# Performance work log

Hardware: AMD Instinct MI355X
Metric: run time of the kernel (lower is better)

## Reference

```python
import jax, jax.numpy as jnp
import numpy as np

B, S, D, H = 4, 1024, 1024, 16
HD = D // H  # head dim 64
EPS = 1e-12

def setup_inputs() -> dict:
    key = jax.random.key(0)
    ks = jax.random.split(key, 10)
    sc = 1.0 / np.sqrt(D)
    return {
        "eeg": jax.random.normal(ks[0], (B, S, D), jnp.float32),
        "pic": jax.random.normal(ks[1], (B, S, D), jnp.float32),
        "Wk": jax.random.normal(ks[2], (D, D), jnp.float32) * sc,
        "bk": jnp.zeros((D,), jnp.float32),
        "Wq": jax.random.normal(ks[3], (D, D), jnp.float32) * sc,
        "bq": jnp.zeros((D,), jnp.float32),
        "Wv": jax.random.normal(ks[4], (D, D), jnp.float32) * sc,
        "bv": jnp.zeros((D,), jnp.float32),
        "Wd": jax.random.normal(ks[5], (D, D), jnp.float32) * sc,
        "bd": jnp.zeros((D,), jnp.float32),
        "ln_w": jnp.ones((D,), jnp.float32),
        "ln_b": jnp.zeros((D,), jnp.float32),
    }

def _heads(x):  # [B,S,D] -> [B,H,S,HD]
    return x.reshape(B, S, H, HD).transpose(0, 2, 1, 3)

def reference(eeg, pic, Wk, bk, Wq, bq, Wv, bv, Wd, bd, ln_w, ln_b):
    k = _heads(eeg @ Wk + bk)
    q = _heads(pic @ Wq + bq)
    v = _heads(pic @ Wv + bv)
    scores = jnp.einsum('bhqd,bhkd->bhqk', q, k) / jnp.sqrt(jnp.float32(HD))
    probs = jax.nn.softmax(scores, axis=-1)  # dropout = identity (eval mode)
    ctx = jnp.einsum('bhqk,bhkd->bhqd', probs, v)
    ctx = ctx.transpose(0, 2, 1, 3).reshape(B, S, D)
    h = ctx @ Wd + bd  # out_dropout = identity (eval)
    x = h + pic
    u = x.mean(-1, keepdims=True)
    s = ((x - u) ** 2).mean(-1, keepdims=True)
    x = (x - u) / jnp.sqrt(s + EPS)
    return ln_w * x + ln_b
```

## Files before the change

### kernel.cpp

```cpp
#include <hip/hip_runtime.h>
#include <hip/hip_bf16.h>

#define BB 4
#define SS 1024
#define DD 1024
#define HH 16
#define HD 64
#define MM (BB * SS)
#define LN_EPS 1e-12f

typedef unsigned short u16;
typedef __attribute__((ext_vector_type(8))) short bf16x8;
typedef __attribute__((ext_vector_type(4))) float f32x4;
typedef __attribute__((ext_vector_type(4))) unsigned short u16x4;
typedef __attribute__((ext_vector_type(8))) unsigned short u16x8;

__device__ __forceinline__ u16 f2bf(float f) {
    __hip_bfloat16 h = __float2bfloat16(f);
    u16 r; __builtin_memcpy(&r, &h, 2); return r;
}
__device__ __forceinline__ float bf2f(u16 u) {
    unsigned v = ((unsigned)u) << 16;
    float f; __builtin_memcpy(&f, &v, 4); return f;
}

typedef const __attribute__((address_space(1))) unsigned int* gas1_t;
typedef __attribute__((address_space(3))) unsigned int* las3_t;
__device__ __forceinline__ void gload16(const void* g, void* s) {
    __builtin_amdgcn_global_load_lds((gas1_t)g, (las3_t)s, 16, 0, 0);
}

__device__ __forceinline__ void vmw0() {
    asm volatile("s_waitcnt vmcnt(0)" ::: "memory");
    __builtin_amdgcn_sched_barrier(0);
}
__device__ __forceinline__ void vmw2() {
    asm volatile("s_waitcnt vmcnt(2)" ::: "memory");
    __builtin_amdgcn_sched_barrier(0);
}
__device__ __forceinline__ void vmw4() {
    asm volatile("s_waitcnt vmcnt(4)" ::: "memory");
    __builtin_amdgcn_sched_barrier(0);
}

__global__ __launch_bounds__(256) void conv2_bf16(
    const float* __restrict__ a, const float* __restrict__ c,
    u16* __restrict__ oa, u16* __restrict__ oc)
{
    const float* in = blockIdx.y ? c : a;
    u16* out = blockIdx.y ? oc : oa;
    size_t i = ((size_t)blockIdx.x * 256 + threadIdx.x) * 8;
    float4 x = *(const float4*)(in + i);
    float4 y = *(const float4*)(in + i + 4);
    u16x8 o;
    o[0]=f2bf(x.x); o[1]=f2bf(x.y); o[2]=f2bf(x.z); o[3]=f2bf(x.w);
    o[4]=f2bf(y.x); o[5]=f2bf(y.y); o[6]=f2bf(y.z); o[7]=f2bf(y.w);
    *(u16x8*)(out + i) = o;
}

__global__ __launch_bounds__(256) void transpose_w4(
    const float* __restrict__ W0, const float* __restrict__ W1,
    const float* __restrict__ W2, const float* __restrict__ W3,
    u16* __restrict__ T0, u16* __restrict__ T1,
    u16* __restrict__ T2, u16* __restrict__ T3)
{
    const int z = blockIdx.z;
    const float* W = (z==0)?W0:(z==1)?W1:(z==2)?W2:W3;
    u16* Wt = (z==0)?T0:(z==1)?T1:(z==2)?T2:T3;

    __shared__ float Ls[64][65];
    const int t = threadIdx.x;
    const int k0 = blockIdx.x * 64, n0 = blockIdx.y * 64;
    #pragma unroll
    for (int i = 0; i < 4; ++i) {
        int r = (t >> 4) + i * 16, c = (t & 15) * 4;
        float4 v = *(const float4*)&W[(size_t)(k0 + r) * DD + n0 + c];
        Ls[r][c] = v.x; Ls[r][c+1] = v.y; Ls[r][c+2] = v.z; Ls[r][c+3] = v.w;
    }
    __syncthreads();
    #pragma unroll
    for (int i = 0; i < 2; ++i) {
        int n = (t >> 3) + i * 32, kc = (t & 7) * 8;
        u16x8 o;
        #pragma unroll
        for (int j = 0; j < 8; ++j) o[j] = f2bf(Ls[kc + j][n]);
        *(u16x8*)&Wt[(size_t)(n0 + n) * DD + k0 + kc] = o;
    }
}

template<int TRANS>
__device__ __forceinline__ void do_phase(
    const u16* Lcur, int wm, int wn, int g, int lr, int mh, int kh, f32x4* acc)
{
    const char* base = (const char*)Lcur;
    bf16x8 af[4], bfr[4];
    #pragma unroll
    for (int i = 0; i < 4; ++i) {
        int row = wm * 128 + mh * 64 + i * 16 + lr;
        af[i] = *(const bf16x8*)(base + row * 128 + ((kh * 4 + g) ^ (row & 7)) * 16);
    }
    #pragma unroll
    for (int i = 0; i < 4; ++i) {
        int row = wn * 64 + i * 16 + lr;
        bfr[i] = *(const bf16x8*)(base + 32768 + row * 128 + ((kh * 4 + g) ^ (row & 7)) * 16);
    }
    __builtin_amdgcn_s_setprio(1);
    #pragma unroll
    for (int i = 0; i < 4; ++i)
        #pragma unroll
        for (int j = 0; j < 4; ++j) {
            int mi = mh * 4 + i;
            if (TRANS)
                acc[j * 8 + mi] = __builtin_amdgcn_mfma_f32_16x16x32_bf16(
                    bfr[j], af[i], acc[j * 8 + mi], 0, 0, 0);
            else
                acc[mi * 4 + j] = __builtin_amdgcn_mfma_f32_16x16x32_bf16(
                    af[i], bfr[j], acc[mi * 4 + j], 0, 0, 0);
        }
    __builtin_amdgcn_s_setprio(0);
}

template<int TRANS>
__device__ __forceinline__ void gemm256_8ph(
    const u16* __restrict__ A, const u16* __restrict__ Bt,
    int bm, int bn, u16* Ls, f32x4* acc)
{
    const int tid = threadIdx.x;
    const int w = tid >> 6, l = tid & 63, g = l >> 4, lr = l & 15;
    const int wm = w >> 2, wn = w & 3;

    const int srow = tid >> 3;
    const int sgc = (tid & 7) ^ (srow & 7);
    const u16* Ag = A + (size_t)(bm + srow) * DD + sgc * 8;
    const u16* Bg = Bt + (size_t)(bn + srow) * DD + sgc * 8;

#define STA(buf, r, k0) gload16(Ag + (size_t)(r) * 64 * DD + (k0), (buf) + (r) * 4096 + w * 512)
#define STB(buf, r, k0) gload16(Bg + (size_t)(r) * 64 * DD + (k0), (buf) + 16384 + (r) * 4096 + w * 512)

    STB(Ls, 0, 0); STB(Ls, 1, 0);
    STB(Ls, 2, 0); STB(Ls, 3, 0);
    STA(Ls, 0, 0); STA(Ls, 2, 0);
    STA(Ls, 1, 0); STA(Ls, 3, 0);

    #pragma unroll 2
    for (int t = 0; t < 16; ++t) {
        const int cur = t & 1;
        const u16* cb = Ls + cur * 32768;
        u16* nb = Ls + (cur ^ 1) * 32768;
        const int nk = (t + 1) * 64;
        const bool last = (t == 15);

        vmw2();
        __builtin_amdgcn_s_barrier();
        if (!last) { STB(nb, 0, nk); STB(nb, 1, nk); }
        do_phase<TRANS>(cb, wm, wn, g, lr, 0, 0, acc);

        __builtin_amdgcn_s_barrier();
        if (!last) { STB(nb, 2, nk); STB(nb, 3, nk); }
        do_phase<TRANS>(cb, wm, wn, g, lr, 0, 1, acc);

        if (last) vmw0(); else vmw4();
        __builtin_amdgcn_s_barrier();
        if (!last) { STA(nb, 0, nk); STA(nb, 2, nk); }
        do_phase<TRANS>(cb, wm, wn, g, lr, 1, 0, acc);

        __builtin_amdgcn_s_barrier();
        if (!last) { STA(nb, 1, nk); STA(nb, 3, nk); }
        do_phase<TRANS>(cb, wm, wn, g, lr, 1, 1, acc);
    }
#undef STA
#undef STB
}

__global__ __launch_bounds__(512, 2) void gemm_qkv(
    const u16* __restrict__ Ae, const u16* __restrict__ Ap,
    const u16* __restrict__ Bk, const u16* __restrict__ Bq, const u16* __restrict__ Bv,
    const float* __restrict__ bk, const float* __restrict__ bq, const float* __restrict__ bv,
    u16* __restrict__ Kb, u16* __restrict__ Qb, u16* __restrict__ VtG)
{
    const int i = (int)blockIdx.x;
    const int x = i & 7, j = i >> 3;
    const int sel = j >> 3, inner = j & 7;
    const int bm = (x * 2 + (inner & 1)) * 256;
    const int bn = (inner >> 1) * 256;

    const u16* A  = sel ? Ap : Ae;
    const u16* Bt = (sel == 0) ? Bk : (sel == 1) ? Bq : Bv;
    const float* bias = (sel == 0) ? bk : (sel == 1) ? bq : bv;
    const float alpha = (sel == 1) ? 0.180336880111120f : 1.0f;

    __shared__ __align__(16) u16 Ls[2 * 32768];

    f32x4 acc[32];
    #pragma unroll
    for (int k = 0; k < 32; ++k) { f32x4 z = {0,0,0,0}; acc[k] = z; }

    const int tid = threadIdx.x;
    const int w = tid >> 6, l = tid & 63, g = l >> 4, lr = l & 15;
    const int wm = w >> 2, wn = w & 3;

    if (sel == 2) {
        gemm256_8ph<1>(A, Bt, bm, bn, Ls, acc);
        #pragma unroll
        for (int ni = 0; ni < 4; ++ni)
            #pragma unroll
            for (int r = 0; r < 4; ++r) {
                int n = bn + wn * 64 + ni * 16 + g * 4 + r;
                float bb = bias[n];
                #pragma unroll
                for (int mi = 0; mi < 8; ++mi) {
                    int m = bm + wm * 128 + mi * 16 + lr;
                    VtG[(size_t)n * MM + m] = f2bf(acc[ni * 8 + mi][r] + bb);
                }
            }
    } else {
        gemm256_8ph<0>(A, Bt, bm, bn, Ls, acc);
        u16* C = sel ? Qb : Kb;
        float b4[4];
        #pragma unroll
        for (int ni = 0; ni < 4; ++ni) b4[ni] = bias[bn + wn * 64 + ni * 16 + lr];
        #pragma unroll
        for (int mi = 0; mi < 8; ++mi)
            #pragma unroll
            for (int ni = 0; ni < 4; ++ni)
                #pragma unroll
                for (int r = 0; r < 4; ++r) {
                    int row = bm + wm * 128 + mi * 16 + g * 4 + r;
                    int col = bn + wn * 64 + ni * 16 + lr;
                    C[(size_t)row * DD + col] = f2bf(alpha * (acc[mi * 4 + ni][r] + b4[ni]));
                }
    }
}

template<int TRANS>
__device__ __forceinline__ void gemm128_loop(
    const u16* __restrict__ A, const u16* __restrict__ Bt,
    int bm, int bn, u16* As, u16* Bs, f32x4 (&acc)[4][4])
{
    const int tid = threadIdx.x;
    const int w = tid >> 6, l = tid & 63, g = l >> 4, lr = l & 15;
    const int wm = w >> 1, wn = w & 1;

    const int srow = tid >> 3, ss = tid & 7;
    const int sgc = ss ^ (srow & 7);
    const u16* Ag = A + (size_t)(bm + srow) * DD + sgc * 8;
    const u16* Bg = Bt + (size_t)(bn + srow) * DD + sgc * 8;

    for (int k0 = 0; k0 < DD; k0 += 64) {
        #pragma unroll
        for (int rr = 0; rr < 4; ++rr)
            gload16(Ag + (size_t)rr * 32 * DD + k0, As + (rr * 256 + w * 64) * 8);
        #pragma unroll
        for (int rr = 0; rr < 4; ++rr)
            gload16(Bg + (size_t)rr * 32 * DD + k0, Bs + (rr * 256 + w * 64) * 8);
        __syncthreads();

        #pragma unroll
        for (int kh = 0; kh < 2; ++kh) {
            bf16x8 af[4], bfr[4];
            #pragma unroll
            for (int mi = 0; mi < 4; ++mi) {
                int row = wm * 64 + mi * 16 + lr;
                af[mi] = *(const bf16x8*)((const char*)As + row * 128 +
                                          ((kh * 4 + g) ^ (row & 7)) * 16);
            }
            #pragma unroll
            for (int ni = 0; ni < 4; ++ni) {
                int row = wn * 64 + ni * 16 + lr;
                bfr[ni] = *(const bf16x8*)((const char*)Bs + row * 128 +
                                           ((kh * 4 + g) ^ (row & 7)) * 16);
            }
            #pragma unroll
            for (int mi = 0; mi < 4; ++mi)
                #pragma unroll
                for (int ni = 0; ni < 4; ++ni) {
                    if (TRANS)
                        acc[ni][mi] = __builtin_amdgcn_mfma_f32_16x16x32_bf16(
                            bfr[ni], af[mi], acc[ni][mi], 0, 0, 0);
                    else
                        acc[mi][ni] = __builtin_amdgcn_mfma_f32_16x16x32_bf16(
                            af[mi], bfr[ni], acc[mi][ni], 0, 0, 0);
                }
        }
        __syncthreads();
    }
}

__global__ __launch_bounds__(256) void gemm_plain(
    const u16* __restrict__ A, const u16* __restrict__ Bt,
    const float* __restrict__ bias, u16* __restrict__ C)
{
    const int i = (int)blockIdx.x;
    const int x = i & 7, j = i >> 3;
    const int bn = (j >> 2) * 128;
    const int bm = (x * 4 + (j & 3)) * 128;

    __shared__ __align__(16) u16 As[128 * 64];
    __shared__ __align__(16) u16 Bs[128 * 64];

    f32x4 acc[4][4];
    #pragma unroll
    for (int a = 0; a < 4; ++a)
        #pragma unroll
        for (int b = 0; b < 4; ++b) { f32x4 z = {0,0,0,0}; acc[a][b] = z; }

    gemm128_loop<0>(A, Bt, bm, bn, As, Bs, acc);

    const int tid = threadIdx.x;
    const int w = tid >> 6, l = tid & 63, g = l >> 4, lr = l & 15;
    const int wm = w >> 1, wn = w & 1;
    float b4[4];
    #pragma unroll
    for (int ni = 0; ni < 4; ++ni) b4[ni] = bias[bn + wn * 64 + ni * 16 + lr];
    #pragma unroll
    for (int mi = 0; mi < 4; ++mi)
        #pragma unroll
        for (int ni = 0; ni < 4; ++ni)
            #pragma unroll
            for (int r = 0; r < 4; ++r) {
                int row = bm + wm * 64 + mi * 16 + g * 4 + r;
                int col = bn + wn * 64 + ni * 16 + lr;
                C[(size_t)row * DD + col] = f2bf(acc[mi][ni][r] + b4[ni]);
            }
}

__global__ __launch_bounds__(512) void attn_mfma(
    const u16* __restrict__ Q, const u16* __restrict__ K,
    const u16* __restrict__ Vt, u16* __restrict__ O)
{
    const int tid = threadIdx.x;
    const int w = tid >> 6, l = tid & 63, g = l >> 4, lr = l & 15;
    int bid = (int)blockIdx.x;
    bid = (bid & 7) * 64 + (bid >> 3);
    const int qb = bid & 7, h = (bid >> 3) & 15, b = bid >> 7;
    const size_t qrow0 = (size_t)b * SS + qb * 128;
    const size_t kv0 = (size_t)b * SS;
    const int hc = h * HD;

    __shared__ __align__(16) u16 Ks[2][64 * 64];
    __shared__ __align__(16) u16 Vs[2][64 * 64];
    __shared__ __align__(16) u16 Ps[8][16 * 72];

    const int srow = tid >> 3, ss = tid & 7;
    const int sgc = ss ^ (srow & 7);
    const u16* kg = K + (kv0 + srow) * DD + hc + sgc * 8;
    const u16* vg = Vt + (size_t)(hc + srow) * MM + kv0 + sgc * 8;

    bf16x8 qf[2];
    {
        const u16* qp = Q + (qrow0 + w * 16 + lr) * DD + hc + g * 8;
        qf[0] = *(const bf16x8*)(qp);
        qf[1] = *(const bf16x8*)(qp + 32);
    }

    f32x4 acc[4];
    #pragma unroll
    for (int dt = 0; dt < 4; ++dt) { f32x4 z = {0,0,0,0}; acc[dt] = z; }
    float m_run = -1e30f, l_run = 0.f;

    gload16(kg, &Ks[0][w * 512]);
    gload16(vg, &Vs[0][w * 512]);
    __syncthreads();

    for (int kb = 0; kb < SS / 64; ++kb) {
        const int cur = kb & 1;
        if (kb < SS / 64 - 1) {
            gload16(kg + (size_t)(kb + 1) * 64 * DD, &Ks[cur ^ 1][w * 512]);
            gload16(vg + (size_t)(kb + 1) * 64, &Vs[cur ^ 1][w * 512]);
        }
        const char* kbase = (const char*)&Ks[cur][0];
        const char* vbase = (const char*)&Vs[cur][0];

        f32x4 st[4];
        __builtin_amdgcn_s_setprio(1);
        #pragma unroll
        for (int kt = 0; kt < 4; ++kt) {
            int row = kt * 16 + lr;
            const char* rb = kbase + row * 128;
            bf16x8 k0 = *(const bf16x8*)(rb + ((0 + g) ^ (row & 7)) * 16);
            bf16x8 k1 = *(const bf16x8*)(rb + ((4 + g) ^ (row & 7)) * 16);
            f32x4 z = {0,0,0,0};
            z = __builtin_amdgcn_mfma_f32_16x16x32_bf16(k0, qf[0], z, 0, 0, 0);
            z = __builtin_amdgcn_mfma_f32_16x16x32_bf16(k1, qf[1], z, 0, 0, 0);
            st[kt] = z;
        }
        __builtin_amdgcn_s_setprio(0);

        float tmax = -1e30f;
        #pragma unroll
        for (int kt = 0; kt < 4; ++kt)
            #pragma unroll
            for (int r = 0; r < 4; ++r) tmax = fmaxf(tmax, st[kt][r]);
        tmax = fmaxf(tmax, __shfl_xor(tmax, 16));
        tmax = fmaxf(tmax, __shfl_xor(tmax, 32));

        if (!__all(tmax <= m_run + 8.f)) {
            float m_new = fmaxf(m_run, tmax);
            float sc = exp2f(m_run - m_new);
            m_run = m_new;
            l_run *= sc;
            float scq[4];
            #pragma unroll
            for (int r = 0; r < 4; ++r) scq[r] = __shfl(sc, g * 4 + r);
            #pragma unroll
            for (int dt = 0; dt < 4; ++dt)
                #pragma unroll
                for (int r = 0; r < 4; ++r) acc[dt][r] *= scq[r];
        }

        float p[16];
        float ps = 0.f;
        #pragma unroll
        for (int kt = 0; kt < 4; ++kt)
            #pragma unroll
            for (int r = 0; r < 4; ++r) {
                float v = exp2f(st[kt][r] - m_run);
                p[kt * 4 + r] = v;
                ps += v;
            }
        ps += __shfl_xor(ps, 16);
        ps += __shfl_xor(ps, 32);
        l_run += ps;

        #pragma unroll
        for (int kt = 0; kt < 4; ++kt) {
            u16x4 h4;
            #pragma unroll
            for (int r = 0; r < 4; ++r) h4[r] = f2bf(p[kt * 4 + r]);
            *(u16x4*)((char*)&Ps[w][0] + lr * 144 + kt * 32 + g * 8) = h4;
        }

        __builtin_amdgcn_s_setprio(1);
        #pragma unroll
        for (int kh = 0; kh < 2; ++kh) {
            bf16x8 pf = *(const bf16x8*)((const char*)&Ps[w][0] + lr * 144 +
                                         kh * 64 + g * 16);
            #pragma unroll
            for (int dt = 0; dt < 4; ++dt) {
                int row = dt * 16 + lr;
                bf16x8 vf = *(const bf16x8*)(vbase + row * 128 +
                                             ((kh * 4 + g) ^ (row & 7)) * 16);
                acc[dt] = __builtin_amdgcn_mfma_f32_16x16x32_bf16(pf, vf, acc[dt], 0, 0, 0);
            }
        }
        __builtin_amdgcn_s_setprio(0);

        __syncthreads();
    }

    float invl[4];
    #pragma unroll
    for (int r = 0; r < 4; ++r) invl[r] = 1.f / __shfl(l_run, g * 4 + r);
    #pragma unroll
    for (int dt = 0; dt < 4; ++dt)
        #pragma unroll
        for (int r = 0; r < 4; ++r) {
            size_t row = qrow0 + w * 16 + g * 4 + r;
            O[row * DD + hc + dt * 16 + lr] = f2bf(acc[dt][r] * invl[r]);
        }
}

__global__ __launch_bounds__(256) void ln_kernel(
    const u16* __restrict__ Hs, const float* __restrict__ P,
    const float* __restrict__ w, const float* __restrict__ bshift,
    float* __restrict__ out)
{
    const int row = blockIdx.x;
    const int tid = threadIdx.x;
    const size_t off = (size_t)row * DD;
    const int c0 = tid * 4;

    u16x4 h4 = *(const u16x4*)&Hs[off + c0];
    float4 p4 = *(const float4*)&P[off + c0];
    float x[4];
    x[0] = bf2f(h4[0]) + p4.x; x[1] = bf2f(h4[1]) + p4.y;
    x[2] = bf2f(h4[2]) + p4.z; x[3] = bf2f(h4[3]) + p4.w;

    float s = x[0] + x[1] + x[2] + x[3];
    #pragma unroll
    for (int o = 32; o >= 1; o >>= 1) s += __shfl_xor(s, o, 64);

    __shared__ float r1[4], r2[4];
    const int wid = tid >> 6;
    if ((tid & 63) == 0) r1[wid] = s;
    __syncthreads();
    const float mean = (r1[0] + r1[1] + r1[2] + r1[3]) * (1.f / (float)DD);

    float d2 = 0.f;
    #pragma unroll
    for (int i = 0; i < 4; ++i) { float d = x[i] - mean; d2 += d * d; }
    #pragma unroll
    for (int o = 32; o >= 1; o >>= 1) d2 += __shfl_xor(d2, o, 64);
    if ((tid & 63) == 0) r2[wid] = d2;
    __syncthreads();
    const float var = (r2[0] + r2[1] + r2[2] + r2[3]) * (1.f / (float)DD);
    const float inv = rsqrtf(var + LN_EPS);

    float4 o4;
    o4.x = w[c0 + 0] * ((x[0] - mean) * inv) + bshift[c0 + 0];
    o4.y = w[c0 + 1] * ((x[1] - mean) * inv) + bshift[c0 + 1];
    o4.z = w[c0 + 2] * ((x[2] - mean) * inv) + bshift[c0 + 2];
    o4.w = w[c0 + 3] * ((x[3] - mean) * inv) + bshift[c0 + 3];
    *(float4*)&out[off + c0] = o4;
}

extern "C" void kernel_launch(void* const* d_in, const int* in_sizes, int n_in,
                              void* d_out, int out_size, void* d_ws, size_t ws_size,
                              hipStream_t stream)
{
    const float* eeg = (const float*)d_in[0];
    const float* pic = (const float*)d_in[1];
    const float* Wk  = (const float*)d_in[2];
    const float* bk  = (const float*)d_in[3];
    const float* Wq  = (const float*)d_in[4];
    const float* bq  = (const float*)d_in[5];
    const float* Wv  = (const float*)d_in[6];
    const float* bv  = (const float*)d_in[7];
    const float* Wd  = (const float*)d_in[8];
    const float* bd  = (const float*)d_in[9];
    const float* lnw = (const float*)d_in[10];
    const float* lnb = (const float*)d_in[11];
    float* out = (float*)d_out;

    u16* ws = (u16*)d_ws;
    const size_t M4 = (size_t)1 << 22;
    u16* Ae  = ws;
    u16* Ap  = ws + M4;
    u16* WtK = ws + 2 * M4;
    u16* WtQ = WtK + (1u << 20);
    u16* WtV = WtQ + (1u << 20);
    u16* WtD = WtV + (1u << 20);
    u16* Kb  = ws + 3 * M4;
    u16* Qb  = ws + 4 * M4;
    u16* VtG = ws + 5 * M4;
    u16* Cb  = ws + 6 * M4;
    u16* Hb  = ws + 7 * M4;

    conv2_bf16<<<dim3(2048, 2), 256, 0, stream>>>(eeg, pic, Ae, Ap);
    transpose_w4<<<dim3(16, 16, 4), 256, 0, stream>>>(Wk, Wq, Wv, Wd,
                                                      WtK, WtQ, WtV, WtD);

    gemm_qkv<<<192, 512, 0, stream>>>(Ae, Ap, WtK, WtQ, WtV,
                                      bk, bq, bv, Kb, Qb, VtG);

    attn_mfma<<<BB * HH * (SS / 128), 512, 0, stream>>>(Qb, Kb, VtG, Cb);

    gemm_plain<<<256, 256, 0, stream>>>(Cb, WtD, bd, Hb);

    ln_kernel<<<MM, 256, 0, stream>>>(Hb, pic, lnw, lnb, out);
}
```

Baseline: 112.8 us.

## Triple-buffer K/V tiles and software-pipeline QK^T ahead of softmax in attention

The attention loop moves from double to triple buffering of K/V tiles in shared memory, prefetching two tiles ahead. The QK^T MFMA for the next tile is issued before the softmax and PV of the current tile, so matrix work can overlap the exp and reduction work. The full __syncthreads at the end of each iteration becomes a single vmcnt wait plus barrier, and the loop is fully unrolled. The P staging buffer now uses an XOR swizzle instead of row padding to avoid LDS bank conflicts. In exchange it uses more LDS and more registers for the second score buffer, which may reduce occupancy.

```diff
diff --git a/kernel.cpp b/kernel.cpp
--- a/kernel.cpp
+++ b/kernel.cpp
@@ -324,6 +324,24 @@
             }
 }
 
+__device__ __forceinline__ void qk_tile(
+    f32x4 (&st)[4], const u16* kbuf, const bf16x8 (&qf)[2], int g, int lr)
+{
+    __builtin_amdgcn_s_setprio(1);
+    #pragma unroll
+    for (int kt = 0; kt < 4; ++kt) {
+        int row = kt * 16 + lr;
+        const char* rb = (const char*)kbuf + row * 128;
+        bf16x8 k0 = *(const bf16x8*)(rb + ((0 + g) ^ (row & 7)) * 16);
+        bf16x8 k1 = *(const bf16x8*)(rb + ((4 + g) ^ (row & 7)) * 16);
+        f32x4 z = {0,0,0,0};
+        z = __builtin_amdgcn_mfma_f32_16x16x32_bf16(k0, qf[0], z, 0, 0, 0);
+        z = __builtin_amdgcn_mfma_f32_16x16x32_bf16(k1, qf[1], z, 0, 0, 0);
+        st[kt] = z;
+    }
+    __builtin_amdgcn_s_setprio(0);
+}
+
 __global__ __launch_bounds__(512) void attn_mfma(
     const u16* __restrict__ Q, const u16* __restrict__ K,
     const u16* __restrict__ Vt, u16* __restrict__ O)
@@ -337,14 +355,18 @@
     const size_t kv0 = (size_t)b * SS;
     const int hc = h * HD;
 
-    __shared__ __align__(16) u16 Ks[2][64 * 64];
-    __shared__ __align__(16) u16 Vs[2][64 * 64];
-    __shared__ __align__(16) u16 Ps[8][16 * 72];
+    __shared__ __align__(16) u16 Ks[3][4096];
+    __shared__ __align__(16) u16 Vs[3][4096];
+    __shared__ __align__(16) u16 Ps[8][1024];
 
     const int srow = tid >> 3, ss = tid & 7;
     const int sgc = ss ^ (srow & 7);
     const u16* kg = K + (kv0 + srow) * DD + hc + sgc * 8;
     const u16* vg = Vt + (size_t)(hc + srow) * MM + kv0 + sgc * 8;
+
+#define STG(t) do { \
+    gload16(kg + (size_t)(t) * 64 * DD, &Ks[(t) % 3][w * 512]); \
+    gload16(vg + (size_t)(t) * 64,      &Vs[(t) % 3][w * 512]); } while (0)
 
     bf16x8 qf[2];
     {
@@ -358,39 +380,29 @@
     for (int dt = 0; dt < 4; ++dt) { f32x4 z = {0,0,0,0}; acc[dt] = z; }
     float m_run = -1e30f, l_run = 0.f;
 
-    gload16(kg, &Ks[0][w * 512]);
-    gload16(vg, &Vs[0][w * 512]);
-    __syncthreads();
-
-    for (int kb = 0; kb < SS / 64; ++kb) {
-        const int cur = kb & 1;
-        if (kb < SS / 64 - 1) {
-            gload16(kg + (size_t)(kb + 1) * 64 * DD, &Ks[cur ^ 1][w * 512]);
-            gload16(vg + (size_t)(kb + 1) * 64, &Vs[cur ^ 1][w * 512]);
-        }
-        const char* kbase = (const char*)&Ks[cur][0];
-        const char* vbase = (const char*)&Vs[cur][0];
-
-        f32x4 st[4];
-        __builtin_amdgcn_s_setprio(1);
-        #pragma unroll
-        for (int kt = 0; kt < 4; ++kt) {
-            int row = kt * 16 + lr;
-            const char* rb = kbase + row * 128;
-            bf16x8 k0 = *(const bf16x8*)(rb + ((0 + g) ^ (row & 7)) * 16);
-            bf16x8 k1 = *(const bf16x8*)(rb + ((4 + g) ^ (row & 7)) * 16);
-            f32x4 z = {0,0,0,0};
-            z = __builtin_amdgcn_mfma_f32_16x16x32_bf16(k0, qf[0], z, 0, 0, 0);
-            z = __builtin_amdgcn_mfma_f32_16x16x32_bf16(k1, qf[1], z, 0, 0, 0);
-            st[kt] = z;
-        }
-        __builtin_amdgcn_s_setprio(0);
+    STG(0); STG(1);
+    vmw2();
+    __builtin_amdgcn_s_barrier();
+
+    f32x4 st[2][4];
+    qk_tile(st[0], &Ks[0][0], qf, g, lr);
+
+    #pragma unroll
+    for (int t = 0; t < 16; ++t) {
+        const int cur = t & 1;
+
+        if (t < 15) {
+            vmw0();
+            __builtin_amdgcn_s_barrier();
+            qk_tile(st[cur ^ 1], &Ks[(t + 1) % 3][0], qf, g, lr);
+            if (t + 2 < 16) STG(t + 2);
+        }
 
         float tmax = -1e30f;
         #pragma unroll
         for (int kt = 0; kt < 4; ++kt)
             #pragma unroll
-            for (int r = 0; r < 4; ++r) tmax = fmaxf(tmax, st[kt][r]);
+            for (int r = 0; r < 4; ++r) tmax = fmaxf(tmax, st[cur][kt][r]);
         tmax = fmaxf(tmax, __shfl_xor(tmax, 16));
         tmax = fmaxf(tmax, __shfl_xor(tmax, 32));
 
@@ -414,7 +426,7 @@
         for (int kt = 0; kt < 4; ++kt)
             #pragma unroll
             for (int r = 0; r < 4; ++r) {
-                float v = exp2f(st[kt][r] - m_run);
+                float v = exp2f(st[cur][kt][r] - m_run);
                 p[kt * 4 + r] = v;
                 ps += v;
             }
@@ -427,14 +439,16 @@
             u16x4 h4;
             #pragma unroll
             for (int r = 0; r < 4; ++r) h4[r] = f2bf(p[kt * 4 + r]);
-            *(u16x4*)((char*)&Ps[w][0] + lr * 144 + kt * 32 + g * 8) = h4;
-        }
-
+            int ch = (2 * kt + (g >> 1)) ^ (lr & 7);
+            *(u16x4*)((char*)&Ps[w][0] + lr * 128 + ch * 16 + (g & 1) * 8) = h4;
+        }
+
+        const char* vbase = (const char*)&Vs[t % 3][0];
         __builtin_amdgcn_s_setprio(1);
         #pragma unroll
         for (int kh = 0; kh < 2; ++kh) {
-            bf16x8 pf = *(const bf16x8*)((const char*)&Ps[w][0] + lr * 144 +
-                                         kh * 64 + g * 16);
+            bf16x8 pf = *(const bf16x8*)((const char*)&Ps[w][0] + lr * 128 +
+                                         (((4 * kh + g) ^ (lr & 7))) * 16);
             #pragma unroll
             for (int dt = 0; dt < 4; ++dt) {
                 int row = dt * 16 + lr;
@@ -444,9 +458,8 @@
             }
         }
         __builtin_amdgcn_s_setprio(0);
-
-        __syncthreads();
-    }
+    }
+#undef STG
 
     float invl[4];
     #pragma unroll
```

New measurement: 111.1 us. Within noise of the previous version (-1.5%).

## Pass softmax probabilities via lane shuffles instead of LDS, restructure K/V prefetch sync

Applied to the files above, without the earlier changes.

The attention kernel no longer writes the bf16 probability tile to shared memory and reads it back. It packs the values into 32-bit words and redistributes them across lanes with shuffles to form the MFMA A operands directly. The per-iteration __syncthreads is replaced by an explicit vmcnt wait plus s_barrier placed before issuing the next prefetch, and launch bounds now request higher occupancy. This cuts LDS traffic and a barrier per tile, at the cost of more shuffle instructions and register pressure.

```diff
diff --git a/kernel.cpp b/kernel.cpp
--- a/kernel.cpp
+++ b/kernel.cpp
@@ -10,10 +10,12 @@
 #define LN_EPS 1e-12f
 
 typedef unsigned short u16;
+typedef unsigned int u32;
 typedef __attribute__((ext_vector_type(8))) short bf16x8;
 typedef __attribute__((ext_vector_type(4))) float f32x4;
 typedef __attribute__((ext_vector_type(4))) unsigned short u16x4;
 typedef __attribute__((ext_vector_type(8))) unsigned short u16x8;
+typedef __attribute__((ext_vector_type(4))) unsigned int u32x4;
 
 __device__ __forceinline__ u16 f2bf(float f) {
     __hip_bfloat16 h = __float2bfloat16(f);
@@ -324,7 +326,7 @@
             }
 }
 
-__global__ __launch_bounds__(512) void attn_mfma(
+__global__ __launch_bounds__(512, 8) void attn_mfma(
     const u16* __restrict__ Q, const u16* __restrict__ K,
     const u16* __restrict__ Vt, u16* __restrict__ O)
 {
@@ -337,14 +339,19 @@
     const size_t kv0 = (size_t)b * SS;
     const int hc = h * HD;
 
-    __shared__ __align__(16) u16 Ks[2][64 * 64];
-    __shared__ __align__(16) u16 Vs[2][64 * 64];
-    __shared__ __align__(16) u16 Ps[8][16 * 72];
+    __shared__ __align__(16) u16 Ks[2][4096];
+    __shared__ __align__(16) u16 Vs[2][4096];
 
     const int srow = tid >> 3, ss = tid & 7;
     const int sgc = ss ^ (srow & 7);
     const u16* kg = K + (kv0 + srow) * DD + hc + sgc * 8;
     const u16* vg = Vt + (size_t)(hc + srow) * MM + kv0 + sgc * 8;
+
+#define STG(t) do { \
+    gload16(kg + (size_t)(t) * 64 * DD, &Ks[(t) & 1][w * 512]); \
+    gload16(vg + (size_t)(t) * 64,      &Vs[(t) & 1][w * 512]); } while (0)
+
+    STG(0);
 
     bf16x8 qf[2];
     {
@@ -358,18 +365,17 @@
     for (int dt = 0; dt < 4; ++dt) { f32x4 z = {0,0,0,0}; acc[dt] = z; }
     float m_run = -1e30f, l_run = 0.f;
 
-    gload16(kg, &Ks[0][w * 512]);
-    gload16(vg, &Vs[0][w * 512]);
-    __syncthreads();
-
-    for (int kb = 0; kb < SS / 64; ++kb) {
-        const int cur = kb & 1;
-        if (kb < SS / 64 - 1) {
-            gload16(kg + (size_t)(kb + 1) * 64 * DD, &Ks[cur ^ 1][w * 512]);
-            gload16(vg + (size_t)(kb + 1) * 64, &Vs[cur ^ 1][w * 512]);
-        }
-        const char* kbase = (const char*)&Ks[cur][0];
-        const char* vbase = (const char*)&Vs[cur][0];
+    const int src0 = lr + ((l & 16) ? 32 : 0);
+    const int src1 = src0 + 16;
+    const bool hi2 = (l & 32) != 0;
+
+    for (int t = 0; t < 16; ++t) {
+        vmw0();
+        __builtin_amdgcn_s_barrier();
+        if (t < 15) STG(t + 1);
+
+        const char* kbase = (const char*)&Ks[t & 1][0];
+        const char* vbase = (const char*)&Vs[t & 1][0];
 
         f32x4 st[4];
         __builtin_amdgcn_s_setprio(1);
@@ -408,45 +414,50 @@
                 for (int r = 0; r < 4; ++r) acc[dt][r] *= scq[r];
         }
 
-        float p[16];
+        u32 A0w[4], A1w[4];
         float ps = 0.f;
         #pragma unroll
-        for (int kt = 0; kt < 4; ++kt)
-            #pragma unroll
-            for (int r = 0; r < 4; ++r) {
-                float v = exp2f(st[kt][r] - m_run);
-                p[kt * 4 + r] = v;
-                ps += v;
-            }
+        for (int kt = 0; kt < 4; ++kt) {
+            float p0 = exp2f(st[kt][0] - m_run);
+            float p1 = exp2f(st[kt][1] - m_run);
+            float p2 = exp2f(st[kt][2] - m_run);
+            float p3 = exp2f(st[kt][3] - m_run);
+            ps += (p0 + p1) + (p2 + p3);
+            u32 w0 = (u32)f2bf(p0) | ((u32)f2bf(p1) << 16);
+            u32 w1 = (u32)f2bf(p2) | ((u32)f2bf(p3) << 16);
+            u32 a0 = (u32)__shfl((int)w0, src0);
+            u32 a1 = (u32)__shfl((int)w1, src0);
+            u32 b0 = (u32)__shfl((int)w0, src1);
+            u32 b1 = (u32)__shfl((int)w1, src1);
+            if (kt == 0) { if (!hi2) { A0w[0]=a0; A0w[1]=a1; A0w[2]=b0; A0w[3]=b1; } }
+            if (kt == 1) { if (hi2)  { A0w[0]=a0; A0w[1]=a1; A0w[2]=b0; A0w[3]=b1; } }
+            if (kt == 2) { if (!hi2) { A1w[0]=a0; A1w[1]=a1; A1w[2]=b0; A1w[3]=b1; } }
+            if (kt == 3) { if (hi2)  { A1w[0]=a0; A1w[1]=a1; A1w[2]=b0; A1w[3]=b1; } }
+        }
         ps += __shfl_xor(ps, 16);
         ps += __shfl_xor(ps, 32);
         l_run += ps;
 
-        #pragma unroll
-        for (int kt = 0; kt < 4; ++kt) {
-            u16x4 h4;
-            #pragma unroll
-            for (int r = 0; r < 4; ++r) h4[r] = f2bf(p[kt * 4 + r]);
-            *(u16x4*)((char*)&Ps[w][0] + lr * 144 + kt * 32 + g * 8) = h4;
+        bf16x8 pf0, pf1;
+        {
+            u32x4 t0 = {A0w[0], A0w[1], A0w[2], A0w[3]};
+            u32x4 t1 = {A1w[0], A1w[1], A1w[2], A1w[3]};
+            __builtin_memcpy(&pf0, &t0, 16);
+            __builtin_memcpy(&pf1, &t1, 16);
         }
 
         __builtin_amdgcn_s_setprio(1);
         #pragma unroll
-        for (int kh = 0; kh < 2; ++kh) {
-            bf16x8 pf = *(const bf16x8*)((const char*)&Ps[w][0] + lr * 144 +
-                                         kh * 64 + g * 16);
-            #pragma unroll
-            for (int dt = 0; dt < 4; ++dt) {
-                int row = dt * 16 + lr;
-                bf16x8 vf = *(const bf16x8*)(vbase + row * 128 +
-                                             ((kh * 4 + g) ^ (row & 7)) * 16);
-                acc[dt] = __builtin_amdgcn_mfma_f32_16x16x32_bf16(pf, vf, acc[dt], 0, 0, 0);
-            }
+        for (int dt = 0; dt < 4; ++dt) {
+            int row = dt * 16 + lr;
+            bf16x8 v0 = *(const bf16x8*)(vbase + row * 128 + ((0 + g) ^ (row & 7)) * 16);
+            bf16x8 v1 = *(const bf16x8*)(vbase + row * 128 + ((4 + g) ^ (row & 7)) * 16);
+            acc[dt] = __builtin_amdgcn_mfma_f32_16x16x32_bf16(pf0, v0, acc[dt], 0, 0, 0);
+            acc[dt] = __builtin_amdgcn_mfma_f32_16x16x32_bf16(pf1, v1, acc[dt], 0, 0, 0);
         }
         __builtin_amdgcn_s_setprio(0);
-
-        __syncthreads();
-    }
+    }
+#undef STG
 
     float invl[4];
     #pragma unroll
```

Result: slower. 140.9 us (+25.0%).
